# Kernel tuning notes

Measured on AMD Instinct MI355X. Metric: run time of the kernel, lower is better.

## Reference

```python
import jax, jax.numpy as jnp
import numpy as np

N_NODES = 100000
N_EDGES = 3200000
IN_CH, HID, OUT_CH = 11, 64, 1


def setup_inputs() -> dict:
    key = jax.random.key(0)
    ks = jax.random.split(key, 10)
    x = jax.random.normal(ks[0], (N_NODES, IN_CH), dtype=jnp.float32)
    edge_index = jax.random.randint(ks[1], (2, N_EDGES), 0, N_NODES, dtype=jnp.int64)
    s = lambda k, shape, fan_in: jax.random.normal(k, shape, jnp.float32) * (1.0 / np.sqrt(fan_in))
    return {
        "x": x,
        "edge_index": edge_index,
        # conv1: lin_l acts on aggregated neighbors (has bias), lin_r on root (no bias)
        "Wl1": s(ks[2], (HID, IN_CH), IN_CH), "bl1": jnp.zeros((HID,), jnp.float32),
        "Wr1": s(ks[3], (HID, IN_CH), IN_CH),
        "Wl2": s(ks[4], (HID, HID), HID), "bl2": jnp.zeros((HID,), jnp.float32),
        "Wr2": s(ks[5], (HID, HID), HID),
        "Wlin": s(ks[6], (OUT_CH, HID), HID), "blin": jnp.zeros((OUT_CH,), jnp.float32),
    }


def _sage_conv(x, src, dst, Wl, bl, Wr):
    # mean aggregation of source features onto destination nodes
    msg = x[src]                                            # [E, d] gather
    agg = jax.ops.segment_sum(msg, dst, num_segments=N_NODES)          # [N, d]
    cnt = jax.ops.segment_sum(jnp.ones_like(dst, jnp.float32), dst, num_segments=N_NODES)
    mean = agg / jnp.maximum(cnt, 1.0)[:, None]             # isolated nodes -> 0
    return mean @ Wl.T + bl + x @ Wr.T


def reference(x, edge_index, Wl1, bl1, Wr1, Wl2, bl2, Wr2, Wlin, blin):
    src, dst = edge_index[0], edge_index[1]
    h = jax.nn.relu(_sage_conv(x, src, dst, Wl1, bl1, Wr1))
    h = jax.nn.relu(_sage_conv(h, src, dst, Wl2, bl2, Wr2))
    return h @ Wlin.T + blin
```

## Files before the change

### kernel.cpp

```cpp
#include <hip/hip_runtime.h>
#include <hip/hip_fp16.h>

#define IN_CH 11
#define HID 64
#define PAD 64
#define OVCAP 16384
#define NBLK 512
#define BSH 7
#define NBKT 782
#define CAP8 768

typedef _Float16 half8_t __attribute__((ext_vector_type(8)));
typedef float f32x4_t __attribute__((ext_vector_type(4)));

__global__ void k_prep(const float* __restrict__ x, const float* __restrict__ Wl2,
                       const float* __restrict__ Wr2, unsigned* __restrict__ xphu,
                       __half* __restrict__ wl2h, __half* __restrict__ wr2h,
                       int* __restrict__ ovcnt, int* __restrict__ bcnt8, int N) {
    int i = blockIdx.x * blockDim.x + threadIdx.x;
    if (i == 0) *ovcnt = 0;
    if (i < 8 * NBKT) bcnt8[i] = 0;
    if (i < HID * HID) {
        wl2h[i] = __float2half_rn(Wl2[i]);
        wr2h[i] = __float2half_rn(Wr2[i]);
    }
    if (i < (N + 1) * 8) {
        int n = i >> 3, j = (i & 7) * 2;
        float a = 0.f, b = 0.f;
        if (n < N) {
            if (j < IN_CH) a = x[n * IN_CH + j];
            if (j + 1 < IN_CH) b = x[n * IN_CH + j + 1];
        }
        unsigned lo = (unsigned)__half_as_ushort(__float2half_rn(a));
        unsigned hi = (unsigned)__half_as_ushort(__float2half_rn(b));
        xphu[i] = lo | (hi << 16);
    }
}

__global__ __launch_bounds__(256) void k_build(const int* __restrict__ src,
        const int* __restrict__ dst, unsigned* __restrict__ ebuf,
        int* __restrict__ bcnt8, int* __restrict__ ovcnt, int* __restrict__ ov,
        int E, int csz) {
    __shared__ int h[NBKT];
    __shared__ int cur[NBKT];
    __shared__ int lim[NBKT];
    int tid = threadIdx.x, blk = blockIdx.x;
    int xcd = blk & 7;
    for (int t = tid; t < NBKT; t += 256) h[t] = 0;
    __syncthreads();
    int c0 = blk * csz, c1 = min(c0 + csz, E);
    for (int base = c0; base < c1; base += 1024) {
        int d[4]; bool ok[4];
        #pragma unroll
        for (int k = 0; k < 4; k++) {
            int e = base + tid + k * 256;
            ok[k] = e < c1;
            d[k] = ok[k] ? dst[e] : 0;
        }
        #pragma unroll
        for (int k = 0; k < 4; k++)
            if (ok[k]) atomicAdd(&h[d[k] >> BSH], 1);
    }
    __syncthreads();
    for (int t = tid; t < NBKT; t += 256) {
        int hc = h[t];
        int cell = xcd * NBKT + t;
        int base = cell * CAP8;
        int off = (hc > 0) ? atomicAdd(&bcnt8[cell], hc) : 0;
        cur[t] = base + off;
        lim[t] = base + CAP8;
    }
    __syncthreads();
    for (int base = c0; base < c1; base += 1024) {
        int d[4], s[4], slot[4];
        bool ok[4];
        #pragma unroll
        for (int k = 0; k < 4; k++) {
            int e = base + tid + k * 256;
            ok[k] = e < c1;
            d[k] = ok[k] ? dst[e] : 0;
            s[k] = ok[k] ? __builtin_nontemporal_load(&src[e]) : 0;
        }
        #pragma unroll
        for (int k = 0; k < 4; k++)
            if (ok[k]) slot[k] = atomicAdd(&cur[d[k] >> BSH], 1);
        #pragma unroll
        for (int k = 0; k < 4; k++) {
            if (!ok[k]) continue;
            if (slot[k] < lim[d[k] >> BSH]) {
                ebuf[slot[k]] = ((unsigned)s[k] << 7) | (unsigned)(d[k] & 127);
            } else {
                int q = atomicAdd(ovcnt, 1);
                if (q < OVCAP) { ov[2 * q] = d[k]; ov[2 * q + 1] = s[k]; }
            }
        }
    }
}

__global__ __launch_bounds__(256) void k_bbuild(const unsigned* __restrict__ ebuf,
        const int* __restrict__ bcnt8,
        int* __restrict__ cnt, int* __restrict__ col64,
        int* __restrict__ ovcnt, int* __restrict__ ov, int N) {
    __shared__ int lc[128];
    __shared__ int colsh[128 * PAD];
    int tid = threadIdx.x, b = blockIdx.x;
    int lo = b << BSH, hi = min(lo + 128, N);
    #pragma unroll
    for (int i = 0; i < 8; i++)
        ((int4*)colsh)[tid + i * 256] = make_int4(N, N, N, N);
    if (tid < 128) lc[tid] = 0;
    __syncthreads();
    for (int x = 0; x < 8; x++) {
        int cell = x * NBKT + b;
        int cc = min(bcnt8[cell], CAP8);
        const unsigned* seg = ebuf + (size_t)cell * CAP8;
        for (int i = tid; i < cc; i += 256) {
            unsigned p = __builtin_nontemporal_load(&seg[i]);
            int row = (int)(p & 127u);
            int sv  = (int)(p >> 7);
            int r = atomicAdd(&lc[row], 1);
            if (r < PAD) {
                colsh[(row << 6) | r] = sv;
            } else {
                int q = atomicAdd(ovcnt, 1);
                if (q < OVCAP) { ov[2 * q] = lo + row; ov[2 * q + 1] = sv; }
            }
        }
    }
    __syncthreads();
    int nn = hi - lo;
    int4* dst4 = (int4*)col64 + (size_t)lo * 16;
    for (int i = tid; i < nn * 16; i += 256) dst4[i] = ((int4*)colsh)[i];
    if (tid < nn) cnt[lo + tid] = lc[tid];
}

__global__ void k_agg1(const unsigned* __restrict__ xphu,
                       const int* __restrict__ col64,
                       float* __restrict__ agg1, int N) {
    int lane = threadIdx.x & 63;
    int n = blockIdx.x * 4 + (threadIdx.x >> 6);
    if (n >= N) return;
    int c8 = lane & 7, sub = lane >> 3;
    const int* cb = col64 + n * PAD;
    int s[8];
    #pragma unroll
    for (int jj = 0; jj < 8; jj++) s[jj] = __builtin_nontemporal_load(&cb[sub + 8 * jj]);
    unsigned v[8];
    #pragma unroll
    for (int jj = 0; jj < 8; jj++) v[jj] = xphu[s[jj] * 8 + c8];
    __half2 a2 = __floats2half2_rn(0.f, 0.f);
    #pragma unroll
    for (int jj = 0; jj < 8; jj++) a2 = __hadd2(a2, *(__half2*)&v[jj]);
    float2 f = __half22float2(a2);
    #pragma unroll
    for (int off = 8; off <= 32; off <<= 1) {
        f.x += __shfl_xor(f.x, off);
        f.y += __shfl_xor(f.y, off);
    }
    if (lane < 8) ((float2*)agg1)[n * 8 + lane] = f;
}

__global__ void k_ov1(const int* __restrict__ ovcnt, const int* __restrict__ ov,
                      const float* __restrict__ x, float* __restrict__ agg1) {
    int c = *ovcnt; if (c > OVCAP) c = OVCAP;
    for (int i = blockIdx.x * blockDim.x + threadIdx.x; i < c;
         i += gridDim.x * blockDim.x) {
        int d = ov[2 * i], s = ov[2 * i + 1];
        for (int ch = 0; ch < IN_CH; ch++)
            atomicAdd(&agg1[d * 16 + ch], x[s * IN_CH + ch]);
    }
}

__global__ void k_dense1(const float* __restrict__ x, const float* __restrict__ agg1,
                         const int* __restrict__ cnt, const float* __restrict__ Wl,
                         const float* __restrict__ bl, const float* __restrict__ Wr,
                         unsigned* __restrict__ h1h, int N) {
    int lane = threadIdx.x & 63;
    int n = blockIdx.x * 4 + (threadIdx.x >> 6);
    if (n > N) return;
    if (n == N) {
        if (lane < 32) h1h[n * 32 + lane] = 0u;
        return;
    }
    int deg = cnt[n];
    float inv = deg > 0 ? 1.f / (float)deg : 0.f;
    float mv = (lane < 16) ? agg1[n * 16 + lane] * inv : 0.f;
    float xv = (lane < IN_CH) ? x[n * IN_CH + lane] : 0.f;
    float h = bl[lane];
    #pragma unroll
    for (int c = 0; c < IN_CH; c++)
        h += Wl[lane * IN_CH + c] * __shfl(mv, c) + Wr[lane * IN_CH + c] * __shfl(xv, c);
    h = fmaxf(h, 0.f);
    unsigned my = (unsigned)__half_as_ushort(__float2half_rn(h));
    unsigned nx = __shfl_down(my, 1);
    if ((lane & 1) == 0) h1h[n * 32 + (lane >> 1)] = my | (nx << 16);
}

__global__ void k_agg2(const uint4* __restrict__ h1h4, const int* __restrict__ col64,
                       float* __restrict__ agg2, int N) {
    int lane = threadIdx.x & 63;
    int n = blockIdx.x * 4 + (threadIdx.x >> 6);
    if (n >= N) return;
    int c8 = lane & 7, sub = lane >> 3;
    const int* cb = col64 + n * PAD;
    int s[8];
    #pragma unroll
    for (int jj = 0; jj < 8; jj++) s[jj] = __builtin_nontemporal_load(&cb[sub + 8 * jj]);
    uint4 v[8];
    #pragma unroll
    for (int jj = 0; jj < 8; jj++) v[jj] = h1h4[s[jj] * 8 + c8];
    __half2 a2[4];
    #pragma unroll
    for (int t = 0; t < 4; t++) a2[t] = __floats2half2_rn(0.f, 0.f);
    #pragma unroll
    for (int jj = 0; jj < 8; jj++) {
        a2[0] = __hadd2(a2[0], *(__half2*)&v[jj].x);
        a2[1] = __hadd2(a2[1], *(__half2*)&v[jj].y);
        a2[2] = __hadd2(a2[2], *(__half2*)&v[jj].z);
        a2[3] = __hadd2(a2[3], *(__half2*)&v[jj].w);
    }
    float acc[8];
    #pragma unroll
    for (int t = 0; t < 4; t++) {
        float2 f = __half22float2(a2[t]);
        acc[2 * t] = f.x; acc[2 * t + 1] = f.y;
    }
    #pragma unroll
    for (int off = 8; off <= 32; off <<= 1) {
        #pragma unroll
        for (int t = 0; t < 8; t++) acc[t] += __shfl_xor(acc[t], off);
    }
    float val = acc[0];
    #pragma unroll
    for (int t = 1; t < 8; t++) if (sub == t) val = acc[t];
    agg2[n * 64 + 8 * c8 + sub] = val;
}

__global__ void k_ov2(const int* __restrict__ ovcnt, const int* __restrict__ ov,
                      const unsigned* __restrict__ h1h, float* __restrict__ agg2) {
    int c = *ovcnt; if (c > OVCAP) c = OVCAP;
    const __half* h1 = (const __half*)h1h;
    for (int i = blockIdx.x * blockDim.x + threadIdx.x; i < c;
         i += gridDim.x * blockDim.x) {
        int d = ov[2 * i], s = ov[2 * i + 1];
        for (int ch = 0; ch < HID; ch++)
            atomicAdd(&agg2[d * 64 + ch], __half2float(h1[s * 64 + ch]));
    }
}

__global__ __launch_bounds__(256) void k_dense2(
    const float4* __restrict__ agg2_4, const int* __restrict__ cnt,
    const uint4* __restrict__ h1h_u4,
    const __half* __restrict__ wl2h, const __half* __restrict__ wr2h,
    const float* __restrict__ bl, const float* __restrict__ Wlin,
    const float* __restrict__ blin, float* __restrict__ out, int N) {
    union U { uint4 u; half8_t h; };
    int lane = threadIdx.x & 63;
    int wave = blockIdx.x * 4 + (threadIdx.x >> 6);
    int nwaves = gridDim.x * 4;
    int r16 = lane & 15, quad = lane >> 4;
    const uint4* wlu = (const uint4*)wl2h;
    const uint4* wru = (const uint4*)wr2h;
    half8_t bfr[4][4];
    #pragma unroll
    for (int tt = 0; tt < 4; tt++) {
        int o = tt * 16 + r16;
        U t0, t1, t2, t3;
        t0.u = wlu[o * 8 + quad];
        t1.u = wlu[o * 8 + 4 + quad];
        t2.u = wru[o * 8 + quad];
        t3.u = wru[o * 8 + 4 + quad];
        bfr[tt][0] = t0.h; bfr[tt][1] = t1.h; bfr[tt][2] = t2.h; bfr[tt][3] = t3.h;
    }
    float bl_c[4], wl_c[4];
    #pragma unroll
    for (int tt = 0; tt < 4; tt++) {
        bl_c[tt] = bl[tt * 16 + r16];
        wl_c[tt] = Wlin[tt * 16 + r16];
    }
    float b0 = blin[0];
    int ntiles = (N + 15) >> 4;
    for (int t = wave; t < ntiles; t += nwaves) {
        int nb = t * 16;
        int n = nb + r16; if (n >= N) n = N - 1;
        int deg = cnt[n];
        float inv = deg > 0 ? 1.f / (float)deg : 0.f;
        float4 m0 = agg2_4[n * 16 + quad * 2];
        float4 m1 = agg2_4[n * 16 + quad * 2 + 1];
        float4 m2 = agg2_4[n * 16 + 8 + quad * 2];
        float4 m3 = agg2_4[n * 16 + 8 + quad * 2 + 1];
        half8_t a0h, a1h;
        a0h[0] = (_Float16)(m0.x * inv); a0h[1] = (_Float16)(m0.y * inv);
        a0h[2] = (_Float16)(m0.z * inv); a0h[3] = (_Float16)(m0.w * inv);
        a0h[4] = (_Float16)(m1.x * inv); a0h[5] = (_Float16)(m1.y * inv);
        a0h[6] = (_Float16)(m1.z * inv); a0h[7] = (_Float16)(m1.w * inv);
        a1h[0] = (_Float16)(m2.x * inv); a1h[1] = (_Float16)(m2.y * inv);
        a1h[2] = (_Float16)(m2.z * inv); a1h[3] = (_Float16)(m2.w * inv);
        a1h[4] = (_Float16)(m3.x * inv); a1h[5] = (_Float16)(m3.y * inv);
        a1h[6] = (_Float16)(m3.z * inv); a1h[7] = (_Float16)(m3.w * inv);
        U a2, a3;
        a2.u = h1h_u4[n * 8 + quad];
        a3.u = h1h_u4[n * 8 + 4 + quad];
        float p0 = 0.f, p1 = 0.f, p2 = 0.f, p3 = 0.f;
        #pragma unroll
        for (int tt = 0; tt < 4; tt++) {
            f32x4_t c = {0.f, 0.f, 0.f, 0.f};
            c = __builtin_amdgcn_mfma_f32_16x16x32_f16(a0h, bfr[tt][0], c, 0, 0, 0);
            c = __builtin_amdgcn_mfma_f32_16x16x32_f16(a1h, bfr[tt][1], c, 0, 0, 0);
            c = __builtin_amdgcn_mfma_f32_16x16x32_f16(a2.h, bfr[tt][2], c, 0, 0, 0);
            c = __builtin_amdgcn_mfma_f32_16x16x32_f16(a3.h, bfr[tt][3], c, 0, 0, 0);
            p0 += fmaxf(c[0] + bl_c[tt], 0.f) * wl_c[tt];
            p1 += fmaxf(c[1] + bl_c[tt], 0.f) * wl_c[tt];
            p2 += fmaxf(c[2] + bl_c[tt], 0.f) * wl_c[tt];
            p3 += fmaxf(c[3] + bl_c[tt], 0.f) * wl_c[tt];
        }
        #pragma unroll
        for (int off = 1; off <= 8; off <<= 1) {
            p0 += __shfl_xor(p0, off); p1 += __shfl_xor(p1, off);
            p2 += __shfl_xor(p2, off); p3 += __shfl_xor(p3, off);
        }
        if (r16 == 0) {
            int nn = nb + quad * 4;
            if (nn + 3 < N) {
                ((float4*)out)[nn >> 2] = make_float4(p0 + b0, p1 + b0, p2 + b0, p3 + b0);
            } else {
                if (nn + 0 < N) out[nn + 0] = p0 + b0;
                if (nn + 1 < N) out[nn + 1] = p1 + b0;
                if (nn + 2 < N) out[nn + 2] = p2 + b0;
                if (nn + 3 < N) out[nn + 3] = p3 + b0;
            }
        }
    }
}


extern "C" void kernel_launch(void* const* d_in, const int* in_sizes, int n_in,
                              void* d_out, int out_size, void* d_ws, size_t ws_size,
                              hipStream_t stream) {
    const float* x    = (const float*)d_in[0];
    const int*   ei   = (const int*)d_in[1];
    const float* Wl1  = (const float*)d_in[2];
    const float* bl1  = (const float*)d_in[3];
    const float* Wr1  = (const float*)d_in[4];
    const float* Wl2  = (const float*)d_in[5];
    const float* bl2  = (const float*)d_in[6];
    const float* Wr2  = (const float*)d_in[7];
    const float* Wlin = (const float*)d_in[8];
    const float* blin = (const float*)d_in[9];
    float* out = (float*)d_out;

    int N = in_sizes[0] / IN_CH;
    int E = in_sizes[1] / 2;
    const int* srcp = ei;
    const int* dstp = ei + E;

    int* ws       = (int*)d_ws;
    int* cnt      = ws;
    int* ovcnt    = ws + N;
    int* col64    = ws + 100032;
    unsigned* xph = (unsigned*)(ws + 6500032);
    unsigned* ebuf= (unsigned*)(ws + 7300064);
    int* bcnt8    = ws + 12104672;
    float* agg1   = (float*)(ws + 7300064);
    float* agg2   = (float*)(ws + 6500032);
    unsigned* h1h = (unsigned*)(ws + 12900096);
    int* ov       = ws + 16100128;
    __half* wl2h  = (__half*)(ws + 16132896);
    __half* wr2h  = (__half*)(ws + 16134944);

    int csz = (E + NBLK - 1) / NBLK;

    k_prep   <<<((N + 1) * 8 + 255) / 256, 256, 0, stream>>>(x, Wl2, Wr2, xph,
                                                             wl2h, wr2h, ovcnt,
                                                             bcnt8, N);
    k_build  <<<NBLK, 256, 0, stream>>>(srcp, dstp, ebuf, bcnt8, ovcnt, ov, E, csz);
    k_bbuild <<<NBKT, 256, 0, stream>>>(ebuf, bcnt8, cnt, col64, ovcnt, ov, N);

    k_agg1   <<<(N + 3) / 4, 256, 0, stream>>>(xph, col64, agg1, N);
    k_ov1    <<<8, 256, 0, stream>>>(ovcnt, ov, x, agg1);
    k_dense1 <<<(N + 4) / 4, 256, 0, stream>>>(x, agg1, cnt, Wl1, bl1, Wr1, h1h, N);

    k_agg2   <<<(N + 3) / 4, 256, 0, stream>>>((const uint4*)h1h, col64, agg2, N);
    k_ov2    <<<8, 256, 0, stream>>>(ovcnt, ov, h1h, agg2);

    k_dense2 <<<512, 256, 0, stream>>>((const float4*)agg2, cnt, (const uint4*)h1h,
                                       wl2h, wr2h, bl2, Wlin, blin, out, N);
}
```

Measured before the change: 263.2 us.

## Skip empty neighbor slots by degree and store normalized layer-2 aggregate as fp16

The padded 64-slot CSR copy and the gather loops in both aggregation kernels now stop at the node degree rounded up to 8, so unused slots are neither written nor read. The layer-2 aggregation applies the mean normalization itself and writes a packed fp16 result, which k_dense2 loads directly as MFMA operands instead of reading fp32 and converting. The overflow kernel now does fp16 atomic adds of pre-scaled values, which may lose accuracy. The stale slots beyond each node's degree are no longer zeroed and rely on the degree guard, and the per-wave branching now varies with degree.

```diff
diff --git a/kernel.cpp b/kernel.cpp
--- a/kernel.cpp
+++ b/kernel.cpp
@@ -130,27 +130,37 @@
     __syncthreads();
     int nn = hi - lo;
     int4* dst4 = (int4*)col64 + (size_t)lo * 16;
-    for (int i = tid; i < nn * 16; i += 256) dst4[i] = ((int4*)colsh)[i];
+    for (int i = tid; i < nn * 16; i += 256) {
+        int row = i >> 4;
+        int sl4 = (i & 15) << 2;
+        int hi8 = min(8, (lc[row] + 7) >> 3) << 3;
+        if (sl4 < hi8) dst4[i] = ((int4*)colsh)[i];
+    }
     if (tid < nn) cnt[lo + tid] = lc[tid];
 }
 
 __global__ void k_agg1(const unsigned* __restrict__ xphu,
-                       const int* __restrict__ col64,
+                       const int* __restrict__ col64, const int* __restrict__ cnt,
                        float* __restrict__ agg1, int N) {
     int lane = threadIdx.x & 63;
     int n = blockIdx.x * 4 + (threadIdx.x >> 6);
     if (n >= N) return;
     int c8 = lane & 7, sub = lane >> 3;
     const int* cb = col64 + n * PAD;
+    int deg = cnt[n];
+    int nj = min(8, (deg + 7) >> 3);
     int s[8];
-    #pragma unroll
-    for (int jj = 0; jj < 8; jj++) s[jj] = __builtin_nontemporal_load(&cb[sub + 8 * jj]);
     unsigned v[8];
     #pragma unroll
-    for (int jj = 0; jj < 8; jj++) v[jj] = xphu[s[jj] * 8 + c8];
+    for (int jj = 0; jj < 8; jj++)
+        if (jj < nj) s[jj] = __builtin_nontemporal_load(&cb[sub + 8 * jj]);
+    #pragma unroll
+    for (int jj = 0; jj < 8; jj++)
+        if (jj < nj) v[jj] = xphu[s[jj] * 8 + c8];
     __half2 a2 = __floats2half2_rn(0.f, 0.f);
     #pragma unroll
-    for (int jj = 0; jj < 8; jj++) a2 = __hadd2(a2, *(__half2*)&v[jj]);
+    for (int jj = 0; jj < 8; jj++)
+        if (jj < nj) a2 = __hadd2(a2, *(__half2*)&v[jj]);
     float2 f = __half22float2(a2);
     #pragma unroll
     for (int off = 8; off <= 32; off <<= 1) {
@@ -197,27 +207,34 @@
 }
 
 __global__ void k_agg2(const uint4* __restrict__ h1h4, const int* __restrict__ col64,
-                       float* __restrict__ agg2, int N) {
+                       const int* __restrict__ cnt, unsigned* __restrict__ agg2h,
+                       int N) {
     int lane = threadIdx.x & 63;
     int n = blockIdx.x * 4 + (threadIdx.x >> 6);
     if (n >= N) return;
     int c8 = lane & 7, sub = lane >> 3;
     const int* cb = col64 + n * PAD;
+    int deg = cnt[n];
+    int nj = min(8, (deg + 7) >> 3);
     int s[8];
-    #pragma unroll
-    for (int jj = 0; jj < 8; jj++) s[jj] = __builtin_nontemporal_load(&cb[sub + 8 * jj]);
     uint4 v[8];
     #pragma unroll
-    for (int jj = 0; jj < 8; jj++) v[jj] = h1h4[s[jj] * 8 + c8];
+    for (int jj = 0; jj < 8; jj++)
+        if (jj < nj) s[jj] = __builtin_nontemporal_load(&cb[sub + 8 * jj]);
+    #pragma unroll
+    for (int jj = 0; jj < 8; jj++)
+        if (jj < nj) v[jj] = h1h4[s[jj] * 8 + c8];
     __half2 a2[4];
     #pragma unroll
     for (int t = 0; t < 4; t++) a2[t] = __floats2half2_rn(0.f, 0.f);
     #pragma unroll
     for (int jj = 0; jj < 8; jj++) {
-        a2[0] = __hadd2(a2[0], *(__half2*)&v[jj].x);
-        a2[1] = __hadd2(a2[1], *(__half2*)&v[jj].y);
-        a2[2] = __hadd2(a2[2], *(__half2*)&v[jj].z);
-        a2[3] = __hadd2(a2[3], *(__half2*)&v[jj].w);
+        if (jj < nj) {
+            a2[0] = __hadd2(a2[0], *(__half2*)&v[jj].x);
+            a2[1] = __hadd2(a2[1], *(__half2*)&v[jj].y);
+            a2[2] = __hadd2(a2[2], *(__half2*)&v[jj].z);
+            a2[3] = __hadd2(a2[3], *(__half2*)&v[jj].w);
+        }
     }
     float acc[8];
     #pragma unroll
@@ -230,27 +247,40 @@
         #pragma unroll
         for (int t = 0; t < 8; t++) acc[t] += __shfl_xor(acc[t], off);
     }
-    float val = acc[0];
-    #pragma unroll
-    for (int t = 1; t < 8; t++) if (sub == t) val = acc[t];
-    agg2[n * 64 + 8 * c8 + sub] = val;
+    if (sub == 0) {
+        float inv = deg > 0 ? 1.f / (float)deg : 0.f;
+        __half2 h0 = __floats2half2_rn(acc[0] * inv, acc[1] * inv);
+        __half2 h1 = __floats2half2_rn(acc[2] * inv, acc[3] * inv);
+        __half2 h2 = __floats2half2_rn(acc[4] * inv, acc[5] * inv);
+        __half2 h3 = __floats2half2_rn(acc[6] * inv, acc[7] * inv);
+        uint4 o;
+        o.x = *(unsigned*)&h0; o.y = *(unsigned*)&h1;
+        o.z = *(unsigned*)&h2; o.w = *(unsigned*)&h3;
+        ((uint4*)agg2h)[n * 8 + c8] = o;
+    }
 }
 
 __global__ void k_ov2(const int* __restrict__ ovcnt, const int* __restrict__ ov,
-                      const unsigned* __restrict__ h1h, float* __restrict__ agg2) {
+                      const unsigned* __restrict__ h1h, const int* __restrict__ cnt,
+                      unsigned* __restrict__ agg2h) {
     int c = *ovcnt; if (c > OVCAP) c = OVCAP;
-    const __half* h1 = (const __half*)h1h;
     for (int i = blockIdx.x * blockDim.x + threadIdx.x; i < c;
          i += gridDim.x * blockDim.x) {
         int d = ov[2 * i], s = ov[2 * i + 1];
-        for (int ch = 0; ch < HID; ch++)
-            atomicAdd(&agg2[d * 64 + ch], __half2float(h1[s * 64 + ch]));
+        int deg = cnt[d];
+        float inv = deg > 0 ? 1.f / (float)deg : 0.f;
+        const __half2* hp = (const __half2*)(h1h + s * 32);
+        __half2* ap = (__half2*)(agg2h + d * 32);
+        for (int ch = 0; ch < 32; ch++) {
+            float2 f = __half22float2(hp[ch]);
+            __half2 adv = __floats2half2_rn(f.x * inv, f.y * inv);
+            unsafeAtomicAdd(&ap[ch], adv);
+        }
     }
 }
 
 __global__ __launch_bounds__(256) void k_dense2(
-    const float4* __restrict__ agg2_4, const int* __restrict__ cnt,
-    const uint4* __restrict__ h1h_u4,
+    const uint4* __restrict__ agg2h4, const uint4* __restrict__ h1h_u4,
     const __half* __restrict__ wl2h, const __half* __restrict__ wr2h,
     const float* __restrict__ bl, const float* __restrict__ Wlin,
     const float* __restrict__ blin, float* __restrict__ out, int N) {
@@ -283,30 +313,17 @@
     for (int t = wave; t < ntiles; t += nwaves) {
         int nb = t * 16;
         int n = nb + r16; if (n >= N) n = N - 1;
-        int deg = cnt[n];
-        float inv = deg > 0 ? 1.f / (float)deg : 0.f;
-        float4 m0 = agg2_4[n * 16 + quad * 2];
-        float4 m1 = agg2_4[n * 16 + quad * 2 + 1];
-        float4 m2 = agg2_4[n * 16 + 8 + quad * 2];
-        float4 m3 = agg2_4[n * 16 + 8 + quad * 2 + 1];
-        half8_t a0h, a1h;
-        a0h[0] = (_Float16)(m0.x * inv); a0h[1] = (_Float16)(m0.y * inv);
-        a0h[2] = (_Float16)(m0.z * inv); a0h[3] = (_Float16)(m0.w * inv);
-        a0h[4] = (_Float16)(m1.x * inv); a0h[5] = (_Float16)(m1.y * inv);
-        a0h[6] = (_Float16)(m1.z * inv); a0h[7] = (_Float16)(m1.w * inv);
-        a1h[0] = (_Float16)(m2.x * inv); a1h[1] = (_Float16)(m2.y * inv);
-        a1h[2] = (_Float16)(m2.z * inv); a1h[3] = (_Float16)(m2.w * inv);
-        a1h[4] = (_Float16)(m3.x * inv); a1h[5] = (_Float16)(m3.y * inv);
-        a1h[6] = (_Float16)(m3.z * inv); a1h[7] = (_Float16)(m3.w * inv);
-        U a2, a3;
+        U a0, a1, a2, a3;
+        a0.u = agg2h4[n * 8 + quad];
+        a1.u = agg2h4[n * 8 + 4 + quad];
         a2.u = h1h_u4[n * 8 + quad];
         a3.u = h1h_u4[n * 8 + 4 + quad];
         float p0 = 0.f, p1 = 0.f, p2 = 0.f, p3 = 0.f;
         #pragma unroll
         for (int tt = 0; tt < 4; tt++) {
             f32x4_t c = {0.f, 0.f, 0.f, 0.f};
-            c = __builtin_amdgcn_mfma_f32_16x16x32_f16(a0h, bfr[tt][0], c, 0, 0, 0);
-            c = __builtin_amdgcn_mfma_f32_16x16x32_f16(a1h, bfr[tt][1], c, 0, 0, 0);
+            c = __builtin_amdgcn_mfma_f32_16x16x32_f16(a0.h, bfr[tt][0], c, 0, 0, 0);
+            c = __builtin_amdgcn_mfma_f32_16x16x32_f16(a1.h, bfr[tt][1], c, 0, 0, 0);
             c = __builtin_amdgcn_mfma_f32_16x16x32_f16(a2.h, bfr[tt][2], c, 0, 0, 0);
             c = __builtin_amdgcn_mfma_f32_16x16x32_f16(a3.h, bfr[tt][3], c, 0, 0, 0);
             p0 += fmaxf(c[0] + bl_c[tt], 0.f) * wl_c[tt];
@@ -362,7 +379,7 @@
     unsigned* ebuf= (unsigned*)(ws + 7300064);
     int* bcnt8    = ws + 12104672;
     float* agg1   = (float*)(ws + 7300064);
-    float* agg2   = (float*)(ws + 6500032);
+    unsigned* agg2h = (unsigned*)(ws + 6500032);
     unsigned* h1h = (unsigned*)(ws + 12900096);
     int* ov       = ws + 16100128;
     __half* wl2h  = (__half*)(ws + 16132896);
@@ -376,13 +393,14 @@
     k_build  <<<NBLK, 256, 0, stream>>>(srcp, dstp, ebuf, bcnt8, ovcnt, ov, E, csz);
     k_bbuild <<<NBKT, 256, 0, stream>>>(ebuf, bcnt8, cnt, col64, ovcnt, ov, N);
 
-    k_agg1   <<<(N + 3) / 4, 256, 0, stream>>>(xph, col64, agg1, N);
+    k_agg1   <<<(N + 3) / 4, 256, 0, stream>>>(xph, col64, cnt, agg1, N);
     k_ov1    <<<8, 256, 0, stream>>>(ovcnt, ov, x, agg1);
     k_dense1 <<<(N + 4) / 4, 256, 0, stream>>>(x, agg1, cnt, Wl1, bl1, Wr1, h1h, N);
 
-    k_agg2   <<<(N + 3) / 4, 256, 0, stream>>>((const uint4*)h1h, col64, agg2, N);
-    k_ov2    <<<8, 256, 0, stream>>>(ovcnt, ov, h1h, agg2);
-
-    k_dense2 <<<512, 256, 0, stream>>>((const float4*)agg2, cnt, (const uint4*)h1h,
+    k_agg2   <<<(N + 3) / 4, 256, 0, stream>>>((const uint4*)h1h, col64, cnt,
+                                               agg2h, N);
+    k_ov2    <<<8, 256, 0, stream>>>(ovcnt, ov, h1h, cnt, agg2h);
+
+    k_dense2 <<<512, 256, 0, stream>>>((const uint4*)agg2h, (const uint4*)h1h,
                                        wl2h, wr2h, bl2, Wlin, blin, out, N);
 }
```

Result: slower. 288.4 us (+9.6%).
